# Kernel optimization log

Hardware: AMD Instinct MI355X
Metric: run time of the kernel (lower is better)

Reference implementation:

```python
import jax, jax.numpy as jnp
import numpy as np

N = 100000
E = 1600000
F = 128
H = 4
D = 32  # emb_dim // heads
C = 2
NEG_SLOPE = 0.2


def setup_inputs() -> dict:
    key = jax.random.key(0)
    ks = jax.random.split(key, 16)
    inp = {
        "x": jax.random.normal(ks[0], (N, F), dtype=jnp.float32),
        "src": jax.random.randint(ks[1], (E,), 0, N, dtype=jnp.int32),
        "dst": jax.random.randint(ks[2], (E,), 0, N, dtype=jnp.int32),
        # layer 1 params (in=F, out=H*D)
        "W1": jax.random.normal(ks[3], (F, H * D), dtype=jnp.float32) * 0.05,
        "al1": jax.random.normal(ks[4], (H, D), dtype=jnp.float32) * 0.05,
        "ar1": jax.random.normal(ks[5], (H, D), dtype=jnp.float32) * 0.05,
        "b1": jnp.zeros((H * D,), dtype=jnp.float32),
        # layer 2 params (in=H*D, out=H*D)
        "W2": jax.random.normal(ks[6], (H * D, H * D), dtype=jnp.float32) * 0.05,
        "al2": jax.random.normal(ks[7], (H, D), dtype=jnp.float32) * 0.05,
        "ar2": jax.random.normal(ks[8], (H, D), dtype=jnp.float32) * 0.05,
        "b2": jnp.zeros((H * D,), dtype=jnp.float32),
        # final classifier
        "Wf": jax.random.normal(ks[9], (H * D, C), dtype=jnp.float32) * 0.05,
        "bf": jnp.zeros((C,), dtype=jnp.float32),
    }
    return inp


def gat_layer(x, src, dst, W, attn_l, attn_r, bias):
    # Linear projection, split into heads: [N, H, D]
    h = (x @ W).reshape(N, H, D)
    # Per-node attention terms: [N, H]
    el = jnp.einsum("nhd,hd->nh", h, attn_l)
    er = jnp.einsum("nhd,hd->nh", h, attn_r)
    # Per-edge logits with LeakyReLU(0.2): [E, H]
    e = jax.nn.leaky_relu(el[src] + er[dst], negative_slope=NEG_SLOPE)
    # Numerically stable edge-softmax over incoming edges of each dst node
    m = jax.ops.segment_max(e, dst, num_segments=N)
    m = jnp.where(jnp.isfinite(m), m, 0.0)  # nodes with no in-edges
    a = jnp.exp(e - m[dst])
    denom = jax.ops.segment_sum(a, dst, num_segments=N)
    alpha = a / jnp.maximum(denom[dst], 1e-9)
    # Weighted message aggregation: scatter-add over dst -> [N, H, D]
    out = jax.ops.segment_sum(h[src] * alpha[:, :, None], dst, num_segments=N)
    out = out + bias.reshape(H, D)
    # is_concat=True: reshape heads into feature dim -> [N, H*D]
    return out.reshape(N, H * D)


def reference(x, src, dst, W1, al1, ar1, b1, W2, al2, ar2, b2, Wf, bf):
    h = gat_layer(x, src, dst, W1, al1, ar1, b1)
    h = gat_layer(h, src, dst, W2, al2, ar2, b2)
    # prediction=True: final linear layer (note: self.activation is never used in forward)
    return h @ Wf + bf
```

## Files before the change

### kernel.cpp

```cpp
#include <hip/hip_runtime.h>
#include <hip/hip_fp16.h>

#define NN 100000
#define EE 1600000
#define NPB 256
#define EPB (EE / NPB)
#define NGRP2 200
#define GR2 (NN / NGRP2)
#define CCAP 10240
#define PSB 50

typedef _Float16 f16x8 __attribute__((ext_vector_type(8)));
typedef float f32x4 __attribute__((ext_vector_type(4)));

__global__ __launch_bounds__(256) void wtrans_k(const float* __restrict__ W,
                                                __half* __restrict__ Wt) {
    int t = blockIdx.x * 256 + threadIdx.x;
    int k = t >> 7, n = t & 127;
    Wt[n * 128 + k] = __float2half(W[k * 128 + n]);
}

template <int INHALF>
__global__ __launch_bounds__(256) void gemm_el_k(const void* __restrict__ Xv,
                                                 const __half* __restrict__ Wt,
                                                 const float* __restrict__ al,
                                                 const float* __restrict__ ar,
                                                 __half* __restrict__ Hout,
                                                 float* __restrict__ el,
                                                 float* __restrict__ er) {
    __shared__ alignas(16) unsigned short Xs[64 * 128];
    __shared__ alignas(16) unsigned short Ws[128 * 128];
    int t = threadIdx.x;
    int row0 = blockIdx.x * 64;

    {
        const uint4* g = (const uint4*)Wt;
#pragma unroll
        for (int j = 0; j < 8; ++j) {
            int c = j * 256 + t;
            uint4 v = g[c];
            int n = c >> 4, kb = (c & 15) << 4;
            *(uint4*)((char*)Ws + n * 256 + (kb ^ ((n & 7) << 4))) = v;
        }
    }
#pragma unroll
    for (int j = 0; j < 4; ++j) {
        int c = j * 256 + t;
        int row = c >> 4, kb = (c & 15) << 4;
        int grow = row0 + row; if (grow >= NN) grow = NN - 1;
        uint4 pk;
        if (INHALF) {
            pk = ((const uint4*)Xv)[(size_t)grow * 16 + (c & 15)];
        } else {
            const float4* xp = (const float4*)Xv + (size_t)grow * 32 + (c & 15) * 2;
            float4 v0 = xp[0], v1 = xp[1];
            __half2 h01 = __floats2half2_rn(v0.x, v0.y);
            __half2 h23 = __floats2half2_rn(v0.z, v0.w);
            __half2 h45 = __floats2half2_rn(v1.x, v1.y);
            __half2 h67 = __floats2half2_rn(v1.z, v1.w);
            pk = make_uint4(__builtin_bit_cast(unsigned, h01),
                            __builtin_bit_cast(unsigned, h23),
                            __builtin_bit_cast(unsigned, h45),
                            __builtin_bit_cast(unsigned, h67));
        }
        *(uint4*)((char*)Xs + row * 256 + (kb ^ ((row & 7) << 4))) = pk;
    }
    __syncthreads();

    int w = t >> 6, lane = t & 63;
    int lr = lane & 15, lg = lane >> 4;
    int arow = w * 16 + lr;

    f32x4 acc[8] = {};
#pragma unroll
    for (int ks = 0; ks < 4; ++ks) {
        int kb = ks * 64 + lg * 16;
        f16x8 a = *(const f16x8*)((char*)Xs + arow * 256 + (kb ^ ((arow & 7) << 4)));
#pragma unroll
        for (int ct = 0; ct < 8; ++ct) {
            int brow = ct * 16 + lr;
            f16x8 b = *(const f16x8*)((char*)Ws + brow * 256 + (kb ^ ((brow & 7) << 4)));
            acc[ct] = __builtin_amdgcn_mfma_f32_16x16x32_f16(a, b, acc[ct], 0, 0, 0);
        }
    }

#pragma unroll
    for (int r = 0; r < 4; ++r) {
        int grow = row0 + w * 16 + lg * 4 + r;
        if (grow < NN) {
            __half* hp = Hout + (size_t)grow * 128 + lr;
#pragma unroll
            for (int ct = 0; ct < 8; ++ct)
                hp[ct * 16] = __float2half(acc[ct][r]);
        }
    }
    float alv[8], arv[8];
#pragma unroll
    for (int ct = 0; ct < 8; ++ct) {
        alv[ct] = al[ct * 16 + lr];
        arv[ct] = ar[ct * 16 + lr];
    }
#pragma unroll
    for (int r = 0; r < 4; ++r) {
        int grow = row0 + w * 16 + lg * 4 + r;
#pragma unroll
        for (int hd = 0; hd < 4; ++hd) {
            float pl = acc[2 * hd][r] * alv[2 * hd] + acc[2 * hd + 1][r] * alv[2 * hd + 1];
            float pr = acc[2 * hd][r] * arv[2 * hd] + acc[2 * hd + 1][r] * arv[2 * hd + 1];
#pragma unroll
            for (int off = 1; off < 16; off <<= 1) {
                pl += __shfl_xor(pl, off, 64);
                pr += __shfl_xor(pr, off, 64);
            }
            if (lr == 0 && grow < NN) {
                el[grow * 4 + hd] = pl;
                er[grow * 4 + hd] = pr;
            }
        }
    }
}

__global__ __launch_bounds__(512) void partA_k(const int* __restrict__ dst,
                                               int* __restrict__ gcnt) {
    __shared__ int cnt[NGRP2];
    int b = blockIdx.x, t = threadIdx.x;
    for (int i = t; i < NGRP2; i += 512) cnt[i] = 0;
    __syncthreads();
    int e_beg = b * EPB;
    for (int e = e_beg + t; e < e_beg + EPB; e += 512)
        atomicAdd(&cnt[dst[e] / GR2], 1);
    __syncthreads();
    for (int i = t; i < NGRP2; i += 512) gcnt[i * NPB + b] = cnt[i];
}

__global__ __launch_bounds__(1024) void psumA_k(const int* __restrict__ gcnt,
                                                int* __restrict__ psum) {
    __shared__ int sh[1024];
    int b = blockIdx.x, t = threadIdx.x;
    sh[t] = gcnt[b * 1024 + t];
    __syncthreads();
    for (int off = 512; off; off >>= 1) {
        if (t < off) sh[t] += sh[t + off];
        __syncthreads();
    }
    if (t == 0) psum[b] = sh[0];
}

__global__ __launch_bounds__(64) void psumB_k(const int* __restrict__ psum,
                                              int* __restrict__ poffb,
                                              int* __restrict__ rowptr) {
    __shared__ int sh[64];
    int t = threadIdx.x;
    int v = (t < PSB) ? psum[t] : 0;
    sh[t] = v;
    __syncthreads();
    for (int off = 1; off < 64; off <<= 1) {
        int u = (t >= off) ? sh[t - off] : 0;
        __syncthreads();
        sh[t] += u;
        __syncthreads();
    }
    if (t < PSB) poffb[t] = sh[t] - v;
    if (t == 0) rowptr[NN] = EE;
}

__global__ __launch_bounds__(1024) void psumC_k(const int* __restrict__ gcnt,
                                                const int* __restrict__ poffb,
                                                int* __restrict__ poff) {
    __shared__ int sh[1024];
    int b = blockIdx.x, t = threadIdx.x;
    int v = gcnt[b * 1024 + t];
    sh[t] = v;
    __syncthreads();
    for (int off = 1; off < 1024; off <<= 1) {
        int u = (t >= off) ? sh[t - off] : 0;
        __syncthreads();
        sh[t] += u;
        __syncthreads();
    }
    poff[b * 1024 + t] = sh[t] - v + poffb[b];
}

__global__ __launch_bounds__(512) void partB_k(const int* __restrict__ src,
                                               const int* __restrict__ dst,
                                               const int* __restrict__ poff,
                                               int2* __restrict__ ebuf) {
    __shared__ int cur[NGRP2];
    int b = blockIdx.x, t = threadIdx.x;
    for (int i = t; i < NGRP2; i += 512) cur[i] = poff[i * NPB + b];
    __syncthreads();
    int e_beg = b * EPB;
    for (int e = e_beg + t; e < e_beg + EPB; e += 512) {
        int d = dst[e], s = src[e];
        int p = atomicAdd(&cur[d / GR2], 1);
        ebuf[p] = make_int2(s, d);
    }
}

__global__ __launch_bounds__(512) void partC_k(const int2* __restrict__ ebuf,
                                               const int* __restrict__ poff,
                                               int* __restrict__ rowptr,
                                               int* __restrict__ csr_src) {
    __shared__ int lsrc[CCAP];
    __shared__ int ldeg[512];
    __shared__ int ssc[512];
    __shared__ int lcur[512];
    int g = blockIdx.x, t = threadIdx.x;
    int nbase = g * GR2;
    int beg = poff[g * NPB];
    int end = (g == NGRP2 - 1) ? EE : poff[(g + 1) * NPB];
    ldeg[t] = 0;
    __syncthreads();
    for (int e = beg + t; e < end; e += 512) {
        int2 sd = ebuf[e];
        atomicAdd(&ldeg[sd.y - nbase], 1);
    }
    __syncthreads();
    int v = ldeg[t];
    ssc[t] = v;
    __syncthreads();
    for (int off = 1; off < 512; off <<= 1) {
        int u = (t >= off) ? ssc[t - off] : 0;
        __syncthreads();
        ssc[t] += u;
        __syncthreads();
    }
    int ex = ssc[t] - v;
    lcur[t] = ex;
    if (t < GR2) rowptr[nbase + t] = beg + ex;
    __syncthreads();
    for (int e = beg + t; e < end; e += 512) {
        int2 sd = ebuf[e];
        int p = atomicAdd(&lcur[sd.y - nbase], 1);
        if (p < CCAP) lsrc[p] = sd.x;
    }
    __syncthreads();
    int len = end - beg; if (len > CCAP) len = CCAP;
    for (int i = t; i < len; i += 512) csr_src[beg + i] = lsrc[i];
}

#define BC16(x, I) __uint_as_float(__builtin_amdgcn_ds_swizzle( \
    __float_as_uint(x), ((I) << 5) | 0x10))

#define AGG_STEP(av, hvp, I)                      \
    {                                             \
        float ai = BC16(av, I);                   \
        float2 f = __half22float2((hvp)[I]);      \
        acc0 = fmaf(ai, f.x, acc0);               \
        acc1 = fmaf(ai, f.y, acc1);               \
    }

#define AGG16(av, hvp)                                                       \
    AGG_STEP(av, hvp, 0)  AGG_STEP(av, hvp, 1)  AGG_STEP(av, hvp, 2)         \
    AGG_STEP(av, hvp, 3)  AGG_STEP(av, hvp, 4)  AGG_STEP(av, hvp, 5)         \
    AGG_STEP(av, hvp, 6)  AGG_STEP(av, hvp, 7)  AGG_STEP(av, hvp, 8)         \
    AGG_STEP(av, hvp, 9)  AGG_STEP(av, hvp, 10) AGG_STEP(av, hvp, 11)        \
    AGG_STEP(av, hvp, 12) AGG_STEP(av, hvp, 13) AGG_STEP(av, hvp, 14)        \
    AGG_STEP(av, hvp, 15)

template <int FINAL>
__global__ __launch_bounds__(64) void gat_agg_k(const int* __restrict__ rowptr,
                                                const int* __restrict__ csr_src,
                                                const float* __restrict__ el,
                                                const float* __restrict__ er,
                                                const __half* __restrict__ h,
                                                const float* __restrict__ bias,
                                                void* __restrict__ outv,
                                                const float* __restrict__ Wf,
                                                const float* __restrict__ bf) {
    int wave = blockIdx.x;
    int lane = threadIdx.x;
    int row = rowptr[wave], end = rowptr[wave + 1];
    int hd = lane >> 4, sub = lane & 15;
    float erd = er[wave * 4 + hd];
    const __half2* hbase = (const __half2*)h + lane;

    float dpart = 0.f, acc0 = 0.f, acc1 = 0.f;
    for (int base = row; base < end; base += 32) {
        int c = end - base;
        int s0 = csr_src[base + (sub < c ? sub : 0)];
        float a0 = 0.f;
        {
            float v = el[s0 * 4 + hd] + erd;
            v = (v >= 0.f) ? v : 0.2f * v;
            if (sub < c) a0 = __expf(v);
        }
        if (c > 16) {
            int i1 = 16 + sub;
            int s1 = csr_src[base + (i1 < c ? i1 : 0)];
            float a1 = 0.f;
            {
                float v = el[s1 * 4 + hd] + erd;
                v = (v >= 0.f) ? v : 0.2f * v;
                if (i1 < c) a1 = __expf(v);
            }
            dpart += a0 + a1;
            __half2 hv[32];
#pragma unroll
            for (int i = 0; i < 16; ++i) {
                int si = __builtin_amdgcn_readlane(s0, i);
                hv[i] = hbase[si * 64];
            }
#pragma unroll
            for (int i = 0; i < 16; ++i) {
                int si = __builtin_amdgcn_readlane(s1, i);
                hv[16 + i] = hbase[si * 64];
            }
            AGG16(a0, hv)
            AGG16(a1, (hv + 16))
        } else {
            dpart += a0;
            __half2 hv[16];
#pragma unroll
            for (int i = 0; i < 16; ++i) {
                int si = __builtin_amdgcn_readlane(s0, i);
                hv[i] = hbase[si * 64];
            }
            AGG16(a0, hv)
        }
    }
    float denom = dpart;
#pragma unroll
    for (int off = 1; off < 16; off <<= 1) denom += __shfl_xor(denom, off, 64);
    float inv = 1.f / fmaxf(denom, 1e-9f);
    float2 bv = *(const float2*)&bias[lane * 2];
    float o0 = acc0 * inv + bv.x;
    float o1 = acc1 * inv + bv.y;

    if (FINAL) {
        float* out = (float*)outv;
        float4 wf = *(const float4*)&Wf[lane * 4];
        float c0 = o0 * wf.x + o1 * wf.z;
        float c1 = o0 * wf.y + o1 * wf.w;
#pragma unroll
        for (int off = 1; off < 64; off <<= 1) {
            c0 += __shfl_xor(c0, off, 64);
            c1 += __shfl_xor(c1, off, 64);
        }
        if (lane == 0) {
            float2 res = make_float2(c0 + bf[0], c1 + bf[1]);
            *(float2*)&out[(size_t)wave * 2] = res;
        }
    } else {
        __half* out = (__half*)outv;
        *(__half2*)&out[(size_t)wave * 128 + lane * 2] = __floats2half2_rn(o0, o1);
    }
}

extern "C" void kernel_launch(void* const* d_in, const int* in_sizes, int n_in,
                              void* d_out, int out_size, void* d_ws, size_t ws_size,
                              hipStream_t stream) {
    const float* x   = (const float*)d_in[0];
    const int*   src = (const int*)d_in[1];
    const int*   dst = (const int*)d_in[2];
    const float* W1  = (const float*)d_in[3];
    const float* al1 = (const float*)d_in[4];
    const float* ar1 = (const float*)d_in[5];
    const float* b1  = (const float*)d_in[6];
    const float* W2  = (const float*)d_in[7];
    const float* al2 = (const float*)d_in[8];
    const float* ar2 = (const float*)d_in[9];
    const float* b2  = (const float*)d_in[10];
    const float* Wf  = (const float*)d_in[11];
    const float* bf  = (const float*)d_in[12];
    float* out = (float*)d_out;

    __half* bufH  = (__half*)d_ws;
    __half* bufO  = bufH + (size_t)NN * 128;
    float* el     = (float*)(bufO + (size_t)NN * 128);
    float* er     = el + NN * 4;
    int* rowptr   = (int*)(er + NN * 4);
    int* csr_src  = rowptr + NN + 2;
    int2* ebuf    = (int2*)(csr_src + EE);
    int* gcnt     = (int*)(ebuf + EE);
    int* poff     = gcnt + NGRP2 * NPB;
    int* psum     = poff + NGRP2 * NPB;
    int* poffb    = psum + PSB;
    __half* Wt1   = (__half*)(poffb + PSB);
    __half* Wt2   = Wt1 + 128 * 128;

    const int T = 256;
    int gGemm = (NN + 63) / 64;

    wtrans_k<<<64, T, 0, stream>>>(W1, Wt1);
    wtrans_k<<<64, T, 0, stream>>>(W2, Wt2);
    partA_k<<<NPB, 512, 0, stream>>>(dst, gcnt);
    psumA_k<<<PSB, 1024, 0, stream>>>(gcnt, psum);
    psumB_k<<<1, 64, 0, stream>>>(psum, poffb, rowptr);
    psumC_k<<<PSB, 1024, 0, stream>>>(gcnt, poffb, poff);
    partB_k<<<NPB, 512, 0, stream>>>(src, dst, poff, ebuf);
    partC_k<<<NGRP2, 512, 0, stream>>>(ebuf, poff, rowptr, csr_src);

    gemm_el_k<0><<<gGemm, T, 0, stream>>>(x, Wt1, al1, ar1, bufH, el, er);
    gat_agg_k<0><<<NN, 64, 0, stream>>>(rowptr, csr_src, el, er, bufH, b1, bufO,
                                        nullptr, nullptr);
    gemm_el_k<1><<<gGemm, T, 0, stream>>>(bufO, Wt2, al2, ar2, bufH, el, er);
    gat_agg_k<1><<<NN, 64, 0, stream>>>(rowptr, csr_src, el, er, bufH, b2, out,
                                        Wf, bf);
}
```

Before: 230.2 us.

## Pack edge buffer to 32-bit, vectorize GEMM epilogue, merge weight transposes

Three changes. The two weight-transpose launches are merged into one kernel. The GEMM swaps its MFMA operands so that each lane holds four consecutive output columns, which allows packed half stores and a float4 attention dot product that needs only two cross-lane shuffles and stores el/er as float4. The partition edge buffer now packs the source index (17 bits) and the local destination offset into one int instead of an int2, halving its write and read traffic in partB and partC. This relies on N < 2^17 and GR2 fitting in the upper bits.

Result: faster. 221.2 us (-3.9%).

```diff
diff --git a/kernel.cpp b/kernel.cpp
--- a/kernel.cpp
+++ b/kernel.cpp
@@ -13,9 +13,14 @@
 typedef _Float16 f16x8 __attribute__((ext_vector_type(8)));
 typedef float f32x4 __attribute__((ext_vector_type(4)));
 
-__global__ __launch_bounds__(256) void wtrans_k(const float* __restrict__ W,
-                                                __half* __restrict__ Wt) {
-    int t = blockIdx.x * 256 + threadIdx.x;
+__global__ __launch_bounds__(256) void wtrans_k(const float* __restrict__ W1,
+                                                const float* __restrict__ W2,
+                                                __half* __restrict__ Wt1,
+                                                __half* __restrict__ Wt2) {
+    int b = blockIdx.x;
+    const float* W = (b & 1) ? W2 : W1;
+    __half* Wt = (b & 1) ? Wt2 : Wt1;
+    int t = (b >> 1) * 256 + threadIdx.x;
     int k = t >> 7, n = t & 127;
     Wt[n * 128 + k] = __float2half(W[k * 128 + n]);
 }
@@ -69,54 +74,55 @@
 
     int w = t >> 6, lane = t & 63;
     int lr = lane & 15, lg = lane >> 4;
-    int arow = w * 16 + lr;
+    int xrow = w * 16 + lr;
 
     f32x4 acc[8] = {};
 #pragma unroll
     for (int ks = 0; ks < 4; ++ks) {
         int kb = ks * 64 + lg * 16;
-        f16x8 a = *(const f16x8*)((char*)Xs + arow * 256 + (kb ^ ((arow & 7) << 4)));
+        f16x8 b = *(const f16x8*)((char*)Xs + xrow * 256 + (kb ^ ((xrow & 7) << 4)));
 #pragma unroll
         for (int ct = 0; ct < 8; ++ct) {
-            int brow = ct * 16 + lr;
-            f16x8 b = *(const f16x8*)((char*)Ws + brow * 256 + (kb ^ ((brow & 7) << 4)));
+            int wrow = ct * 16 + lr;
+            f16x8 a = *(const f16x8*)((char*)Ws + wrow * 256 + (kb ^ ((wrow & 7) << 4)));
             acc[ct] = __builtin_amdgcn_mfma_f32_16x16x32_f16(a, b, acc[ct], 0, 0, 0);
         }
     }
 
-#pragma unroll
-    for (int r = 0; r < 4; ++r) {
-        int grow = row0 + w * 16 + lg * 4 + r;
-        if (grow < NN) {
-            __half* hp = Hout + (size_t)grow * 128 + lr;
-#pragma unroll
-            for (int ct = 0; ct < 8; ++ct)
-                hp[ct * 16] = __float2half(acc[ct][r]);
-        }
-    }
-    float alv[8], arv[8];
+    int grow = row0 + w * 16 + lr;
+    bool valid = grow < NN;
+    if (valid) {
+        __half* hp = Hout + (size_t)grow * 128 + lg * 4;
+#pragma unroll
+        for (int ct = 0; ct < 8; ++ct) {
+            __half2 p0 = __floats2half2_rn(acc[ct][0], acc[ct][1]);
+            __half2 p1 = __floats2half2_rn(acc[ct][2], acc[ct][3]);
+            uint2 pk = make_uint2(__builtin_bit_cast(unsigned, p0),
+                                  __builtin_bit_cast(unsigned, p1));
+            *(uint2*)(hp + ct * 16) = pk;
+        }
+    }
+    float pl[4] = {}, pr[4] = {};
 #pragma unroll
     for (int ct = 0; ct < 8; ++ct) {
-        alv[ct] = al[ct * 16 + lr];
-        arv[ct] = ar[ct * 16 + lr];
-    }
-#pragma unroll
-    for (int r = 0; r < 4; ++r) {
-        int grow = row0 + w * 16 + lg * 4 + r;
-#pragma unroll
-        for (int hd = 0; hd < 4; ++hd) {
-            float pl = acc[2 * hd][r] * alv[2 * hd] + acc[2 * hd + 1][r] * alv[2 * hd + 1];
-            float pr = acc[2 * hd][r] * arv[2 * hd] + acc[2 * hd + 1][r] * arv[2 * hd + 1];
-#pragma unroll
-            for (int off = 1; off < 16; off <<= 1) {
-                pl += __shfl_xor(pl, off, 64);
-                pr += __shfl_xor(pr, off, 64);
-            }
-            if (lr == 0 && grow < NN) {
-                el[grow * 4 + hd] = pl;
-                er[grow * 4 + hd] = pr;
-            }
-        }
+        int hd = ct >> 1;
+        float4 a_l = *(const float4*)&al[ct * 16 + lg * 4];
+        float4 a_r = *(const float4*)&ar[ct * 16 + lg * 4];
+        pl[hd] += acc[ct][0] * a_l.x + acc[ct][1] * a_l.y +
+                  acc[ct][2] * a_l.z + acc[ct][3] * a_l.w;
+        pr[hd] += acc[ct][0] * a_r.x + acc[ct][1] * a_r.y +
+                  acc[ct][2] * a_r.z + acc[ct][3] * a_r.w;
+    }
+#pragma unroll
+    for (int hd = 0; hd < 4; ++hd) {
+        pl[hd] += __shfl_xor(pl[hd], 16, 64);
+        pl[hd] += __shfl_xor(pl[hd], 32, 64);
+        pr[hd] += __shfl_xor(pr[hd], 16, 64);
+        pr[hd] += __shfl_xor(pr[hd], 32, 64);
+    }
+    if (lg == 0 && valid) {
+        *(float4*)&el[grow * 4] = make_float4(pl[0], pl[1], pl[2], pl[3]);
+        *(float4*)&er[grow * 4] = make_float4(pr[0], pr[1], pr[2], pr[3]);
     }
 }
 
@@ -184,7 +190,7 @@
 __global__ __launch_bounds__(512) void partB_k(const int* __restrict__ src,
                                                const int* __restrict__ dst,
                                                const int* __restrict__ poff,
-                                               int2* __restrict__ ebuf) {
+                                               int* __restrict__ ebuf) {
     __shared__ int cur[NGRP2];
     int b = blockIdx.x, t = threadIdx.x;
     for (int i = t; i < NGRP2; i += 512) cur[i] = poff[i * NPB + b];
@@ -192,12 +198,13 @@
     int e_beg = b * EPB;
     for (int e = e_beg + t; e < e_beg + EPB; e += 512) {
         int d = dst[e], s = src[e];
-        int p = atomicAdd(&cur[d / GR2], 1);
-        ebuf[p] = make_int2(s, d);
-    }
-}
-
-__global__ __launch_bounds__(512) void partC_k(const int2* __restrict__ ebuf,
+        int g = d / GR2;
+        int p = atomicAdd(&cur[g], 1);
+        ebuf[p] = s | ((d - g * GR2) << 17);
+    }
+}
+
+__global__ __launch_bounds__(512) void partC_k(const int* __restrict__ ebuf,
                                                const int* __restrict__ poff,
                                                int* __restrict__ rowptr,
                                                int* __restrict__ csr_src) {
@@ -211,10 +218,8 @@
     int end = (g == NGRP2 - 1) ? EE : poff[(g + 1) * NPB];
     ldeg[t] = 0;
     __syncthreads();
-    for (int e = beg + t; e < end; e += 512) {
-        int2 sd = ebuf[e];
-        atomicAdd(&ldeg[sd.y - nbase], 1);
-    }
+    for (int e = beg + t; e < end; e += 512)
+        atomicAdd(&ldeg[ebuf[e] >> 17], 1);
     __syncthreads();
     int v = ldeg[t];
     ssc[t] = v;
@@ -230,9 +235,9 @@
     if (t < GR2) rowptr[nbase + t] = beg + ex;
     __syncthreads();
     for (int e = beg + t; e < end; e += 512) {
-        int2 sd = ebuf[e];
-        int p = atomicAdd(&lcur[sd.y - nbase], 1);
-        if (p < CCAP) lsrc[p] = sd.x;
+        int pk = ebuf[e];
+        int p = atomicAdd(&lcur[pk >> 17], 1);
+        if (p < CCAP) lsrc[p] = pk & 0x1FFFF;
     }
     __syncthreads();
     int len = end - beg; if (len > CCAP) len = CCAP;
@@ -371,8 +376,8 @@
     float* er     = el + NN * 4;
     int* rowptr   = (int*)(er + NN * 4);
     int* csr_src  = rowptr + NN + 2;
-    int2* ebuf    = (int2*)(csr_src + EE);
-    int* gcnt     = (int*)(ebuf + EE);
+    int* ebuf     = csr_src + EE;
+    int* gcnt     = ebuf + EE;
     int* poff     = gcnt + NGRP2 * NPB;
     int* psum     = poff + NGRP2 * NPB;
     int* poffb    = psum + PSB;
@@ -382,8 +387,7 @@
     const int T = 256;
     int gGemm = (NN + 63) / 64;
 
-    wtrans_k<<<64, T, 0, stream>>>(W1, Wt1);
-    wtrans_k<<<64, T, 0, stream>>>(W2, Wt2);
+    wtrans_k<<<128, T, 0, stream>>>(W1, W2, Wt1, Wt2);
     partA_k<<<NPB, 512, 0, stream>>>(dst, gcnt);
     psumA_k<<<PSB, 1024, 0, stream>>>(gcnt, psum);
     psumB_k<<<1, 64, 0, stream>>>(psum, poffb, rowptr);
```
